# Performance work log

Measured on AMD Instinct MI355X. Metric: run time of the kernel, lower is better.

The kernel has to match this reference:

```python
import jax, jax.numpy as jnp
import numpy as np

L = 2048      # sequence length (self.len)
DIM = 1024    # model dim
DPOS = 128    # positional encoding dim
B = 4
EPS = 1e-5


def make_pe(length, d):
    # standard sinusoidal positional encoding, shape [length, d]
    pos = np.arange(length)[:, None].astype(np.float32)
    div = np.exp(-np.arange(0, d, 2).astype(np.float32) * (np.log(10000.0) / d))
    pe = np.zeros((length, d), dtype=np.float32)
    pe[:, 0::2] = np.sin(pos * div)
    pe[:, 1::2] = np.cos(pos * div)
    return jnp.asarray(pe)


def setup_inputs() -> dict:
    key = jax.random.key(0)
    ks = jax.random.split(key, 16)
    s = lambda fan_in: 1.0 / np.sqrt(fan_in)
    inp = {
        "z": jax.random.normal(ks[0], (B, L, DIM), jnp.float32),
        "x": jax.random.normal(ks[1], (B, L, DIM), jnp.float32),
        "a": jax.random.normal(ks[2], (1,), jnp.float32),
        "pe": make_pe(L, DPOS),
        # torch Linear weights stored [out, in]
        "w_pos1": jax.random.normal(ks[3], (DPOS + DIM, DPOS), jnp.float32) * s(DPOS),
        "b_pos1": jnp.zeros((DPOS + DIM,), jnp.float32),
        "w_pos2": jax.random.normal(ks[4], (DIM, DPOS + DIM), jnp.float32) * s(DPOS + DIM),
        "b_pos2": jnp.zeros((DIM,), jnp.float32),
        "w1": jax.random.normal(ks[5], (DIM * 2, DIM), jnp.float32) * s(DIM),
        "b1": jnp.zeros((DIM * 2,), jnp.float32),
        "w2": jax.random.normal(ks[6], (DIM, DIM * 2), jnp.float32) * s(DIM * 2),
        "b2": jnp.zeros((DIM,), jnp.float32),
        "w3": jax.random.normal(ks[7], (DIM * 2, DIM), jnp.float32) * s(DIM),
        "b3": jnp.zeros((DIM * 2,), jnp.float32),
        "w4": jax.random.normal(ks[8], (DIM, DIM * 2), jnp.float32) * s(DIM * 2),
        "b4": jnp.zeros((DIM,), jnp.float32),
        "ln_g": jnp.ones((DIM,), jnp.float32),
        "ln_b": jnp.zeros((DIM,), jnp.float32),
    }
    return inp


def _layer_norm(v, g, b):
    mu = jnp.mean(v, axis=-1, keepdims=True)
    var = jnp.var(v, axis=-1, keepdims=True)
    return (v - mu) * jax.lax.rsqrt(var + EPS) * g + b


def _lin(v, w, b):
    return v @ w.T + b


def reference(z, x, a, pe, w_pos1, b_pos1, w_pos2, b_pos2,
              w1, b1, w2, b2, w3, b3, w4, b4, ln_g, ln_b):
    zn = _layer_norm(z, ln_g, ln_b)                       # [B, L, D]
    fz = jnp.fft.rfft(zn, n=2 * L, axis=1)                # [B, L+1, D] complex
    expa = jnp.exp(a)                                     # [1]
    window = jnp.exp(-jnp.arange(L, dtype=jnp.float32) * expa)  # [L]
    h = _lin(pe, w_pos1, b_pos1)                          # [L, DPOS+D]
    h = jax.nn.gelu(h, approximate=False)
    h = _lin(h, w_pos2, b_pos2)                           # [L, D] (dropout eval = id)
    wfh = jnp.fft.rfft(window[:, None] * h, n=2 * L, axis=0)  # [L+1, D]
    cwhz = jnp.fft.irfft(wfh * fz, axis=1)[:, :L, :]      # [B, L, D]
    x1 = _lin(x, w1, b1)
    x1 = jax.nn.gelu(x1, approximate=False)
    x1 = _lin(x1, w2, b2)
    x1 = x1 * cwhz + z
    y = _layer_norm(x1, ln_g, ln_b)
    y = _lin(y, w3, b3)
    y = jax.nn.gelu(y, approximate=False)
    y = _lin(y, w4, b4)
    return y + x1
```

## Files before the change

kernel.cpp:

```cpp
#include <hip/hip_runtime.h>
#include <hip/hip_bf16.h>
#include <cmath>

typedef __hip_bfloat16 bf16;
typedef __attribute__((ext_vector_type(8))) short bf16x8;
typedef __attribute__((ext_vector_type(4))) float f32x4;

static __device__ __forceinline__ float b2f(bf16 v) { return __bfloat162float(v); }
static __device__ __forceinline__ bf16 f2b(float v) { return __float2bfloat16(v); }
static __device__ __forceinline__ float us2f(unsigned short u) {
  return __uint_as_float(((unsigned)u) << 16);
}

static __device__ __forceinline__ void gl2lds16(const bf16* g, bf16* l) {
  __builtin_amdgcn_global_load_lds(
      (const __attribute__((address_space(1))) void*)g,
      (__attribute__((address_space(3))) void*)l, 16, 0, 0);
}

static __device__ __forceinline__ float gelu_fast(float v) {
  float u = v * (0.7978845608f + 0.0356774081f * v * v);
  float e = __expf(2.f * u);
  return v * (e * __frcp_rn(e + 1.f));
}

struct CvtSegs { const float* src[7]; int blk_off[8]; };
__global__ __launch_bounds__(256) void cvt7_k(CvtSegs s, bf16* __restrict__ dst0)
{
  int b = blockIdx.x;
  int seg = 0;
#pragma unroll
  for (int i = 0; i < 6; ++i) seg += (b >= s.blk_off[i + 1]) ? 1 : 0;
  const float* src = s.src[seg] + (size_t)(b - s.blk_off[seg]) * 1024;
  bf16* dst = dst0 + (size_t)b * 1024;
  int idx = threadIdx.x * 4;
  float4 v = *(const float4*)(src + idx);
  union { bf16 bb[4]; ushort4 u; } o;
  o.bb[0] = f2b(v.x); o.bb[1] = f2b(v.y); o.bb[2] = f2b(v.z); o.bb[3] = f2b(v.w);
  *(ushort4*)(dst + idx) = o.u;
}

__global__ __launch_bounds__(256) void cvt_k(const float* __restrict__ in,
                                             bf16* __restrict__ out, int n)
{
  int idx = (blockIdx.x * 256 + threadIdx.x) * 4;
  if (idx >= n) return;
  float4 v = *(const float4*)(in + idx);
  union { bf16 b[4]; ushort4 u; } o;
  o.b[0] = f2b(v.x); o.b[1] = f2b(v.y); o.b[2] = f2b(v.z); o.b[3] = f2b(v.w);
  *(ushort4*)(out + idx) = o.u;
}

__global__ __launch_bounds__(256) void ln_k(const float* __restrict__ X, bf16* __restrict__ Y,
                                            const float* __restrict__ gamma,
                                            const float* __restrict__ beta)
{
  __shared__ float red[16];
  const int row = blockIdx.x, tid = threadIdx.x;
  float4 v = *(const float4*)(X + (size_t)row * 1024 + tid * 4);
  float s  = v.x + v.y + v.z + v.w;
  float s2 = v.x * v.x + v.y * v.y + v.z * v.z + v.w * v.w;
#pragma unroll
  for (int m = 32; m; m >>= 1) { s += __shfl_xor(s, m, 64); s2 += __shfl_xor(s2, m, 64); }
  const int wid = tid >> 6;
  if ((tid & 63) == 0) { red[wid] = s; red[wid + 8] = s2; }
  __syncthreads();
  s  = red[0] + red[1] + red[2] + red[3];
  s2 = red[8] + red[9] + red[10] + red[11];
  const float mu  = s * (1.f / 1024.f);
  const float var = s2 * (1.f / 1024.f) - mu * mu;
  const float rs  = rsqrtf(var + 1e-5f);
  float4 g = *(const float4*)(gamma + tid * 4);
  float4 bt = *(const float4*)(beta + tid * 4);
  union { bf16 b[4]; ushort4 u; } o;
  o.b[0] = f2b((v.x - mu) * rs * g.x + bt.x);
  o.b[1] = f2b((v.y - mu) * rs * g.y + bt.y);
  o.b[2] = f2b((v.z - mu) * rs * g.z + bt.z);
  o.b[3] = f2b((v.w - mu) * rs * g.w + bt.w);
  *(ushort4*)(Y + (size_t)row * 1024 + tid * 4) = o.u;
}

template<int EPI>
__global__ __launch_bounds__(256, 3) void gemm_k(
    const bf16* __restrict__ A, const bf16* __restrict__ W,
    const float* __restrict__ bias, void* __restrict__ Out,
    const void* __restrict__ aux0, const void* __restrict__ aux1,
    int M, int N, int K)
{
  __shared__ bf16 As[3][128 * 32];
  __shared__ bf16 Bs[3][128 * 32];
  const int tid = threadIdx.x;
  const int wid = tid >> 6, lane = tid & 63;
  const int quad = lane >> 4, l16 = lane & 15;
  const int wm = wid >> 1, wn = wid & 1;

  const int nwg = gridDim.x * gridDim.y;
  int lid = blockIdx.y * gridDim.x + blockIdx.x;
  {
    const int q = nwg >> 3, r = nwg & 7;
    const int xcd = lid & 7, loc = lid >> 3;
    const int base = (xcd < r) ? xcd * (q + 1) : r * (q + 1) + (xcd - r) * q;
    lid = base + loc;
  }
  const int bx = lid % gridDim.x, by = lid / gridDim.x;
  const int m0 = by * 128, n0 = bx * 128;

  f32x4 acc[4][4];
#pragma unroll
  for (int i = 0; i < 4; ++i)
#pragma unroll
    for (int j = 0; j < 4; ++j) acc[i][j] = (f32x4){0.f, 0.f, 0.f, 0.f};

  const bf16 *ga[2], *gb[2];
  int ldso[2];
#pragma unroll
  for (int r = 0; r < 2; ++r) {
    int p = r * 256 + wid * 64 + lane;
    int row = p >> 2;
    int sko = ((p & 3) ^ ((p >> 3) & 3)) << 3;
    ga[r] = A + (size_t)(m0 + row) * K + sko;
    gb[r] = W + (size_t)(n0 + row) * K + sko;
    ldso[r] = (r * 256 + wid * 64) * 8;
  }
  int apos[4], bpos[4];
#pragma unroll
  for (int i = 0; i < 4; ++i) {
    int ar = wm * 64 + i * 16 + l16;
    apos[i] = (ar * 4 + (quad ^ ((ar >> 1) & 3))) * 8;
    int br = wn * 64 + i * 16 + l16;
    bpos[i] = (br * 4 + (quad ^ ((br >> 1) & 3))) * 8;
  }

  const int niter = K >> 5;
#pragma unroll
  for (int t = 0; t < 2; ++t)
#pragma unroll
    for (int r = 0; r < 2; ++r) {
      gl2lds16(ga[r] + t * 32, &As[t][ldso[r]]);
      gl2lds16(gb[r] + t * 32, &Bs[t][ldso[r]]);
    }

  int cur = 0;
  for (int k = 0; k < niter; ++k) {
    if (k == niter - 1) { asm volatile("s_waitcnt vmcnt(0)" ::: "memory"); }
    else               { asm volatile("s_waitcnt vmcnt(4)" ::: "memory"); }
    asm volatile("s_barrier" ::: "memory");

    const bf16* as = As[cur];
    const bf16* bs = Bs[cur];
    bf16x8 af[4], bfr[4];
#pragma unroll
    for (int i = 0; i < 4; ++i) af[i]  = *(const bf16x8*)(as + apos[i]);
#pragma unroll
    for (int j = 0; j < 4; ++j) bfr[j] = *(const bf16x8*)(bs + bpos[j]);
    asm volatile("s_waitcnt lgkmcnt(0)" ::: "memory");

    if (k + 2 < niter) {
      int nb = cur + 2; if (nb >= 3) nb -= 3;
#pragma unroll
      for (int r = 0; r < 2; ++r) {
        gl2lds16(ga[r] + (k + 2) * 32, &As[nb][ldso[r]]);
        gl2lds16(gb[r] + (k + 2) * 32, &Bs[nb][ldso[r]]);
      }
    }
#pragma unroll
    for (int i = 0; i < 4; ++i)
#pragma unroll
      for (int j = 0; j < 4; ++j)
        acc[i][j] = __builtin_amdgcn_mfma_f32_16x16x32_bf16(af[i], bfr[j], acc[i][j], 0, 0, 0);
    cur += 1; if (cur == 3) cur = 0;
  }

  float expa = 0.f;
  if (EPI == 1) expa = expf(((const float*)aux0)[0]);
#pragma unroll
  for (int i = 0; i < 4; ++i) {
    const int gm_base = m0 + wm * 64 + i * 16 + quad * 4;
#pragma unroll
    for (int j = 0; j < 4; ++j) {
      const int gn = n0 + wn * 64 + j * 16 + l16;
      const float bv = bias[gn];
#pragma unroll
      for (int r = 0; r < 4; ++r) {
        const int gm = gm_base + r;
        const size_t off = (size_t)gm * N + gn;
        float v = acc[i][j][r] + bv;
        if (EPI == 0) ((bf16*)Out)[off] = f2b(gelu_fast(v));
        else if (EPI == 1) ((float*)Out)[off] = v * expf(-(float)gm * expa);
        else if (EPI == 2) ((float*)Out)[off] = v * ((const float*)aux0)[off] + ((const float*)aux1)[off];
        else ((float*)Out)[off] = v + ((const float*)aux0)[off];
      }
    }
  }
}

__global__ __launch_bounds__(256) void conv_k(
    const bf16* __restrict__ zn,
    const float* __restrict__ wh,
    const float* __restrict__ a,
    float* __restrict__ out)
{
  __shared__ float whs[64 * 64];
  __shared__ float znt[128 * 64];
  const int tid = threadIdx.x;
  const int dd = tid & 63, ttg = tid >> 6;
  const int t0 = blockIdx.x * 64, d0 = blockIdx.y * 64, b = blockIdx.z;
  const float expa = expf(a[0]);
  const float smax = 20.7f / expa;
  const unsigned short* znu = (const unsigned short*)zn;

  float acc[16];
#pragma unroll
  for (int q = 0; q < 16; ++q) acc[q] = 0.f;

  for (int sb = 0; sb <= t0 + 63; sb += 64) {
    if ((float)sb > smax) break;
    float4 wv4[4];
#pragma unroll
    for (int i = 0; i < 4; ++i) {
      int cc = tid + 256 * i;
      int row = cc >> 4, dq = (cc & 15) * 4;
      wv4[i] = *(const float4*)&wh[(size_t)(sb + row) * 1024 + d0 + dq];
    }
    ushort4 zv4[8];
#pragma unroll
    for (int i = 0; i < 8; ++i) {
      int cc = tid + 256 * i;
      int row = cc >> 4, dq = (cc & 15) * 4;
      int u = t0 - sb - 64 + row;
      zv4[i] = (u >= 0) ? *(const ushort4*)&znu[((size_t)b * 2048 + u) * 1024 + d0 + dq]
                        : make_ushort4(0, 0, 0, 0);
    }
#pragma unroll
    for (int i = 0; i < 4; ++i) {
      int cc = tid + 256 * i;
      *(float4*)&whs[(cc >> 4) * 64 + (cc & 15) * 4] = wv4[i];
    }
#pragma unroll
    for (int i = 0; i < 8; ++i) {
      int cc = tid + 256 * i;
      float4 o;
      o.x = us2f(zv4[i].x); o.y = us2f(zv4[i].y); o.z = us2f(zv4[i].z); o.w = us2f(zv4[i].w);
      *(float4*)&znt[(cc >> 4) * 64 + (cc & 15) * 4] = o;
    }
    __syncthreads();

    float win[16];
#pragma unroll
    for (int q = 0; q < 16; ++q) win[q] = znt[(ttg * 16 + q + 64) * 64 + dd];
#pragma unroll
    for (int ss = 0; ss < 64; ++ss) {
      float wv = whs[ss * 64 + dd];
#pragma unroll
      for (int q = 0; q < 16; ++q) acc[q] += wv * win[q];
      if (ss < 63) {
#pragma unroll
        for (int q = 15; q >= 1; --q) win[q] = win[q - 1];
        win[0] = znt[(ttg * 16 + 63 - ss) * 64 + dd];
      }
    }
    __syncthreads();
  }
#pragma unroll
  for (int q = 0; q < 16; ++q) {
    int t = t0 + ttg * 16 + q;
    out[((size_t)b * 2048 + t) * 1024 + d0 + dd] = acc[q];
  }
}

extern "C" void kernel_launch(void* const* d_in, const int* in_sizes, int n_in,
                              void* d_out, int out_size, void* d_ws, size_t ws_size,
                              hipStream_t stream)
{
  const float* z      = (const float*)d_in[0];
  const float* x      = (const float*)d_in[1];
  const float* a      = (const float*)d_in[2];
  const float* pe     = (const float*)d_in[3];
  const float* w_pos1 = (const float*)d_in[4];
  const float* b_pos1 = (const float*)d_in[5];
  const float* w_pos2 = (const float*)d_in[6];
  const float* b_pos2 = (const float*)d_in[7];
  const float* w1     = (const float*)d_in[8];
  const float* b1     = (const float*)d_in[9];
  const float* w2     = (const float*)d_in[10];
  const float* b2     = (const float*)d_in[11];
  const float* w3     = (const float*)d_in[12];
  const float* b3     = (const float*)d_in[13];
  const float* w4     = (const float*)d_in[14];
  const float* b4     = (const float*)d_in[15];
  const float* ln_g   = (const float*)d_in[16];
  const float* ln_b   = (const float*)d_in[17];

  char* ws = (char*)d_ws;
  bf16* pe_bf  = (bf16*)(ws + 0);
  bf16* wp1_bf = (bf16*)(ws + 524288);
  bf16* wp2_bf = (bf16*)(ws + 819200);
  bf16* w1_bf  = (bf16*)(ws + 3178496);
  bf16* w2_bf  = (bf16*)(ws + 7372800);
  bf16* w3_bf  = (bf16*)(ws + 11567104);
  bf16* w4_bf  = (bf16*)(ws + 15761408);
  bf16* h1     = (bf16*)(ws + 19955712);
  bf16* zn_bf  = (bf16*)(ws + 24674304);
  bf16* x_bf   = (bf16*)(ws + 41451520);
  float* wh    = (float*)(ws + 58228736);
  float* cwhz  = (float*)(ws + 66617344);
  bf16*  x1n   = (bf16*)(ws + 66617344);
  bf16*  g     = (bf16*)(ws + 100171776);
  float* x1    = (float*)(ws + 24674304);
  float* out   = (float*)d_out;

  CvtSegs segs;
  segs.src[0] = pe;  segs.src[1] = w_pos1; segs.src[2] = w_pos2;
  segs.src[3] = w1;  segs.src[4] = w2;     segs.src[5] = w3; segs.src[6] = w4;
  int bo[8] = {0, 256, 400, 1552, 3600, 5648, 7696, 9744};
  for (int i = 0; i < 8; ++i) segs.blk_off[i] = bo[i];
  cvt7_k<<<9744, 256, 0, stream>>>(segs, (bf16*)ws);
  cvt_k<<<8192, 256, 0, stream>>>(x, x_bf, 8388608);

  ln_k<<<8192, 256, 0, stream>>>(z, zn_bf, ln_g, ln_b);
  gemm_k<0><<<dim3(9, 16), 256, 0, stream>>>(pe_bf, wp1_bf, b_pos1, h1, nullptr, nullptr, 2048, 1152, 128);
  gemm_k<1><<<dim3(8, 16), 256, 0, stream>>>(h1, wp2_bf, b_pos2, wh, a, nullptr, 2048, 1024, 1152);
  conv_k<<<dim3(32, 16, 4), 256, 0, stream>>>(zn_bf, wh, a, cwhz);
  gemm_k<0><<<dim3(16, 64), 256, 0, stream>>>(x_bf, w1_bf, b1, g, nullptr, nullptr, 8192, 2048, 1024);
  gemm_k<2><<<dim3(8, 64), 256, 0, stream>>>(g, w2_bf, b2, x1, cwhz, z, 8192, 1024, 2048);
  ln_k<<<8192, 256, 0, stream>>>(x1, x1n, ln_g, ln_b);
  gemm_k<0><<<dim3(16, 64), 256, 0, stream>>>(x1n, w3_bf, b3, g, nullptr, nullptr, 8192, 2048, 1024);
  gemm_k<3><<<dim3(8, 64), 256, 0, stream>>>(g, w4_bf, b4, out, x1, nullptr, 8192, 1024, 2048);
}
```

Baseline: 418.3 us.

## Add 256x256-tile 8-wave GEMM kernel for the two up-projection GEMMs

Introduces a new GEMM kernel with 512 threads, 256x256 output tiles, K-step 64, and double-buffered LDS filled via global_load_lds. The MFMA work is interleaved with barriers and s_setprio in a ping-pong schedule. It replaces the 128x128 kernel for the two 8192x2048x1024 GEMMs with GELU epilogue, aiming for higher data reuse per tile and better overlap of loads with compute. The trade-offs are much higher register and LDS use (128KB LDS), fewer workgroups (256), and scalar bf16 stores in the epilogue.

```diff
diff --git a/kernel.cpp b/kernel.cpp
--- a/kernel.cpp
+++ b/kernel.cpp
@@ -78,6 +78,131 @@
   o.b[2] = f2b((v.z - mu) * rs * g.z + bt.z);
   o.b[3] = f2b((v.w - mu) * rs * g.w + bt.w);
   *(ushort4*)(Y + (size_t)row * 1024 + tid * 4) = o.u;
+}
+
+template<int EPI>
+__global__ __launch_bounds__(512, 2) void gemm8p_k(
+    const bf16* __restrict__ A, const bf16* __restrict__ W,
+    const float* __restrict__ bias, void* __restrict__ Out,
+    int M, int N, int K)
+{
+  __shared__ bf16 lds[65536];
+  const int tid = threadIdx.x;
+  const int wid = tid >> 6, lane = tid & 63;
+  const int quad = lane >> 4, l16 = lane & 15;
+  const int wm = wid >> 2, wn = wid & 3;
+
+  const int nwg = gridDim.x * gridDim.y;
+  int lid = blockIdx.y * gridDim.x + blockIdx.x;
+  {
+    const int q = nwg >> 3, r = nwg & 7;
+    const int xcd = lid & 7, loc = lid >> 3;
+    const int base = (xcd < r) ? xcd * (q + 1) : r * (q + 1) + (xcd - r) * q;
+    lid = base + loc;
+  }
+  const int bx = lid % gridDim.x, by = lid / gridDim.x;
+  const int m0 = by * 256, n0 = bx * 256;
+
+  f32x4 acc[8][4];
+#pragma unroll
+  for (int i = 0; i < 8; ++i)
+#pragma unroll
+    for (int j = 0; j < 4; ++j) acc[i][j] = (f32x4){0.f, 0.f, 0.f, 0.f};
+
+  const int aoff0 = wm * 8192 + quad * 1024 + l16 * 8;
+  const int boff0 = (wn >> 1) * 8192 + quad * 1024 + (wn & 1) * 512 + l16 * 8;
+
+  const int NT = K >> 6;
+
+#define STAGE_TILE(t)                                                              \
+  {                                                                                \
+    bf16* asl = lds + ((t) & 1) * 16384;                                           \
+    bf16* bsl = lds + 32768 + ((t) & 1) * 16384;                                   \
+    const size_t ko = (size_t)(t) * 64 + wid * 8;                                  \
+    _Pragma("unroll")                                                              \
+    for (int H = 0; H < 2; ++H)                                                    \
+      _Pragma("unroll")                                                            \
+      for (int h = 0; h < 2; ++h) {                                                \
+        gl2lds16(A + (size_t)(m0 + H * 128 + h * 64 + lane) * K + ko,              \
+                 asl + H * 8192 + wid * 1024 + h * 512);                           \
+        gl2lds16(W + (size_t)(n0 + H * 128 + h * 64 + lane) * K + ko,              \
+                 bsl + H * 8192 + wid * 1024 + h * 512);                           \
+      }                                                                            \
+  }
+
+  STAGE_TILE(0);
+  asm volatile("s_waitcnt vmcnt(0)" ::: "memory");
+  asm volatile("s_barrier" ::: "memory");
+
+  for (int T = 0; T < NT; ++T) {
+    const bf16* as = lds + (T & 1) * 16384;
+    const bf16* bs = lds + 32768 + (T & 1) * 16384;
+    bf16x8 bf[4][2];
+    bf16x8 af[2][2];
+
+#pragma unroll
+    for (int nf = 0; nf < 4; ++nf)
+#pragma unroll
+      for (int ks = 0; ks < 2; ++ks)
+        bf[nf][ks] = *(const bf16x8*)(bs + boff0 + ks * 4096 + nf * 128);
+#pragma unroll
+    for (int i = 0; i < 2; ++i)
+#pragma unroll
+      for (int ks = 0; ks < 2; ++ks)
+        af[i][ks] = *(const bf16x8*)(as + aoff0 + ks * 4096 + i * 128);
+    if (T + 1 < NT) STAGE_TILE(T + 1);
+    asm volatile("s_barrier" ::: "memory");
+    asm volatile("s_waitcnt lgkmcnt(0)" ::: "memory");
+    __builtin_amdgcn_s_setprio(1);
+#pragma unroll
+    for (int nf = 0; nf < 4; ++nf)
+#pragma unroll
+      for (int i = 0; i < 2; ++i)
+#pragma unroll
+        for (int ks = 0; ks < 2; ++ks)
+          acc[i][nf] = __builtin_amdgcn_mfma_f32_16x16x32_bf16(af[i][ks], bf[nf][ks], acc[i][nf], 0, 0, 0);
+    __builtin_amdgcn_s_setprio(0);
+    asm volatile("s_barrier" ::: "memory");
+
+#pragma unroll
+    for (int q = 1; q < 4; ++q) {
+#pragma unroll
+      for (int i = 0; i < 2; ++i)
+#pragma unroll
+        for (int ks = 0; ks < 2; ++ks)
+          af[i][ks] = *(const bf16x8*)(as + aoff0 + ks * 4096 + (2 * q + i) * 128);
+      if (q == 3) { asm volatile("s_waitcnt vmcnt(0)" ::: "memory"); }
+      asm volatile("s_barrier" ::: "memory");
+      asm volatile("s_waitcnt lgkmcnt(0)" ::: "memory");
+      __builtin_amdgcn_s_setprio(1);
+#pragma unroll
+      for (int nf = 0; nf < 4; ++nf)
+#pragma unroll
+        for (int i = 0; i < 2; ++i)
+#pragma unroll
+          for (int ks = 0; ks < 2; ++ks)
+            acc[2 * q + i][nf] = __builtin_amdgcn_mfma_f32_16x16x32_bf16(af[i][ks], bf[nf][ks], acc[2 * q + i][nf], 0, 0, 0);
+      __builtin_amdgcn_s_setprio(0);
+      asm volatile("s_barrier" ::: "memory");
+    }
+  }
+#undef STAGE_TILE
+
+#pragma unroll
+  for (int mf = 0; mf < 8; ++mf) {
+    const int gm_base = m0 + wm * 128 + mf * 16 + quad * 4;
+#pragma unroll
+    for (int nf = 0; nf < 4; ++nf) {
+      const int gn = n0 + wn * 64 + nf * 16 + l16;
+      const float bv = bias[gn];
+#pragma unroll
+      for (int r = 0; r < 4; ++r) {
+        const size_t off = (size_t)(gm_base + r) * N + gn;
+        float v = acc[mf][nf][r] + bv;
+        ((bf16*)Out)[off] = f2b(gelu_fast(v));
+      }
+    }
+  }
 }
 
 template<int EPI>
@@ -321,9 +446,9 @@
   gemm_k<0><<<dim3(9, 16), 256, 0, stream>>>(pe_bf, wp1_bf, b_pos1, h1, nullptr, nullptr, 2048, 1152, 128);
   gemm_k<1><<<dim3(8, 16), 256, 0, stream>>>(h1, wp2_bf, b_pos2, wh, a, nullptr, 2048, 1024, 1152);
   conv_k<<<dim3(32, 16, 4), 256, 0, stream>>>(zn_bf, wh, a, cwhz);
-  gemm_k<0><<<dim3(16, 64), 256, 0, stream>>>(x_bf, w1_bf, b1, g, nullptr, nullptr, 8192, 2048, 1024);
+  gemm8p_k<0><<<dim3(8, 32), 512, 0, stream>>>(x_bf, w1_bf, b1, g, 8192, 2048, 1024);
   gemm_k<2><<<dim3(8, 64), 256, 0, stream>>>(g, w2_bf, b2, x1, cwhz, z, 8192, 1024, 2048);
   ln_k<<<8192, 256, 0, stream>>>(x1, x1n, ln_g, ln_b);
-  gemm_k<0><<<dim3(16, 64), 256, 0, stream>>>(x1n, w3_bf, b3, g, nullptr, nullptr, 8192, 2048, 1024);
+  gemm8p_k<0><<<dim3(8, 32), 512, 0, stream>>>(x1n, w3_bf, b3, g, 8192, 2048, 1024);
   gemm_k<3><<<dim3(8, 64), 256, 0, stream>>>(g, w4_bf, b4, out, x1, nullptr, 8192, 1024, 2048);
 }
```

Result: slower. 439.2 us (+5.0%).

## Use larger 256-row tiles with 512-thread blocks for the four big GEMMs

Applied to the files above, without the earlier changes.

Adds two GEMM kernels with 512 threads per block and a three-slot pipeline that loads directly from global memory into LDS. The up-projection uses 256x256 tiles and the down-projection uses 256x128 tiles. Both replace the 128x128 kernel for the four large FFN GEMMs, raising data reuse per block and cutting redundant global/L2 traffic. The new LDS layout drops the XOR swizzle, which may add bank conflicts. The grids shrink to 256 blocks, which lowers wave-count flexibility and may cost occupancy. The XCD swizzle is factored into a helper.

```diff
diff --git a/kernel.cpp b/kernel.cpp
--- a/kernel.cpp
+++ b/kernel.cpp
@@ -22,6 +22,13 @@
   float u = v * (0.7978845608f + 0.0356774081f * v * v);
   float e = __expf(2.f * u);
   return v * (e * __frcp_rn(e + 1.f));
+}
+
+static __device__ __forceinline__ int xcd_swz(int lid, int nwg) {
+  const int q = nwg >> 3, r = nwg & 7;
+  const int xcd = lid & 7, loc = lid >> 3;
+  const int base = (xcd < r) ? xcd * (q + 1) : r * (q + 1) + (xcd - r) * q;
+  return base + loc;
 }
 
 struct CvtSegs { const float* src[7]; int blk_off[8]; };
@@ -80,6 +87,199 @@
   *(ushort4*)(Y + (size_t)row * 1024 + tid * 4) = o.u;
 }
 
+__global__ __launch_bounds__(512, 2) void gemm3sa_k(
+    const bf16* __restrict__ A, const bf16* __restrict__ W,
+    const float* __restrict__ bias, bf16* __restrict__ Out,
+    int M, int N, int K)
+{
+  __shared__ bf16 lds[49152];
+  const int tid = threadIdx.x;
+  const int wid = tid >> 6, lane = tid & 63;
+  const int quad = lane >> 4, l16 = lane & 15;
+  const int wm = wid >> 2, wn = wid & 3;
+
+  const int nwg = gridDim.x * gridDim.y;
+  int lid = xcd_swz(blockIdx.y * gridDim.x + blockIdx.x, nwg);
+  const int bx = lid % gridDim.x, by = lid / gridDim.x;
+  const int m0 = by * 256, n0 = bx * 256;
+
+  f32x4 acc[8][4];
+#pragma unroll
+  for (int i = 0; i < 8; ++i)
+#pragma unroll
+    for (int j = 0; j < 4; ++j) acc[i][j] = (f32x4){0.f, 0.f, 0.f, 0.f};
+
+  const bf16 *ga[2], *gb[2];
+  int ldso[2];
+#pragma unroll
+  for (int r = 0; r < 2; ++r) {
+    const int row = (wid & 3) * 64 + lane;
+    const int ch  = 2 * r + (wid >> 2);
+    ga[r] = A + (size_t)(m0 + row) * K + ch * 8;
+    gb[r] = W + (size_t)(n0 + row) * K + ch * 8;
+    ldso[r] = (r * 512 + wid * 64) * 8;
+  }
+  const int aofs = quad * 2048 + wm * 1024 + l16 * 8;
+  const int bofs = quad * 2048 + wn * 512 + l16 * 8;
+
+  const int niter = K >> 5;
+
+#define STAGE_A(kk, slot)                                                   \
+  {                                                                         \
+    bf16* asl = lds + (slot) * 8192;                                        \
+    bf16* bsl = lds + 24576 + (slot) * 8192;                                \
+    _Pragma("unroll")                                                       \
+    for (int r = 0; r < 2; ++r) {                                           \
+      gl2lds16(ga[r] + (kk) * 32, asl + ldso[r]);                           \
+      gl2lds16(gb[r] + (kk) * 32, bsl + ldso[r]);                           \
+    }                                                                       \
+  }
+
+  STAGE_A(0, 0);
+  STAGE_A(1, 1);
+
+  int cur = 0;
+  for (int k = 0; k < niter; ++k) {
+    if (k == niter - 1) { asm volatile("s_waitcnt vmcnt(0)" ::: "memory"); }
+    else               { asm volatile("s_waitcnt vmcnt(4)" ::: "memory"); }
+    asm volatile("s_barrier" ::: "memory");
+
+    const bf16* as = lds + cur * 8192;
+    const bf16* bs = lds + 24576 + cur * 8192;
+    bf16x8 bfr[4], af[8];
+#pragma unroll
+    for (int nf = 0; nf < 4; ++nf) bfr[nf] = *(const bf16x8*)(bs + bofs + nf * 128);
+#pragma unroll
+    for (int mf = 0; mf < 8; ++mf) af[mf]  = *(const bf16x8*)(as + aofs + mf * 128);
+
+    if (k + 2 < niter) {
+      int nb = cur + 2; if (nb >= 3) nb -= 3;
+      STAGE_A(k + 2, nb);
+    }
+#pragma unroll
+    for (int mf = 0; mf < 8; ++mf)
+#pragma unroll
+      for (int nf = 0; nf < 4; ++nf)
+        acc[mf][nf] = __builtin_amdgcn_mfma_f32_16x16x32_bf16(af[mf], bfr[nf], acc[mf][nf], 0, 0, 0);
+    cur += 1; if (cur == 3) cur = 0;
+  }
+#undef STAGE_A
+
+#pragma unroll
+  for (int mf = 0; mf < 8; ++mf) {
+    const int gm_base = m0 + wm * 128 + mf * 16 + quad * 4;
+#pragma unroll
+    for (int nf = 0; nf < 4; ++nf) {
+      const int gn = n0 + wn * 64 + nf * 16 + l16;
+      const float bv = bias[gn];
+#pragma unroll
+      for (int r = 0; r < 4; ++r) {
+        const size_t off = (size_t)(gm_base + r) * N + gn;
+        Out[off] = f2b(gelu_fast(acc[mf][nf][r] + bv));
+      }
+    }
+  }
+}
+
+template<int EPI>
+__global__ __launch_bounds__(512, 2) void gemm3sb_k(
+    const bf16* __restrict__ A, const bf16* __restrict__ W,
+    const float* __restrict__ bias, float* __restrict__ Out,
+    const float* __restrict__ aux0, const float* __restrict__ aux1,
+    int M, int N, int K)
+{
+  __shared__ bf16 lds[36864];
+  const int tid = threadIdx.x;
+  const int wid = tid >> 6, lane = tid & 63;
+  const int quad = lane >> 4, l16 = lane & 15;
+  const int wm = wid >> 1, wn = wid & 1;
+
+  const int nwg = gridDim.x * gridDim.y;
+  int lid = xcd_swz(blockIdx.y * gridDim.x + blockIdx.x, nwg);
+  const int bx = lid % gridDim.x, by = lid / gridDim.x;
+  const int m0 = by * 256, n0 = bx * 128;
+
+  f32x4 acc[4][4];
+#pragma unroll
+  for (int i = 0; i < 4; ++i)
+#pragma unroll
+    for (int j = 0; j < 4; ++j) acc[i][j] = (f32x4){0.f, 0.f, 0.f, 0.f};
+
+  const bf16 *ga[2], *gbp;
+  int ldsoA[2];
+#pragma unroll
+  for (int r = 0; r < 2; ++r) {
+    const int row = (wid & 3) * 64 + lane;
+    const int ch  = 2 * r + (wid >> 2);
+    ga[r] = A + (size_t)(m0 + row) * K + ch * 8;
+    ldsoA[r] = (r * 512 + wid * 64) * 8;
+  }
+  gbp = W + (size_t)(n0 + (wid & 1) * 64 + lane) * K + (wid >> 1) * 8;
+  const int ldsoB = wid * 512;
+
+  const int aofs = quad * 2048 + wm * 512 + l16 * 8;
+  const int bofs = quad * 1024 + wn * 512 + l16 * 8;
+
+  const int niter = K >> 5;
+
+#define STAGE_B(kk, slot)                                                   \
+  {                                                                         \
+    bf16* asl = lds + (slot) * 8192;                                        \
+    bf16* bsl = lds + 24576 + (slot) * 4096;                                \
+    _Pragma("unroll")                                                       \
+    for (int r = 0; r < 2; ++r)                                             \
+      gl2lds16(ga[r] + (kk) * 32, asl + ldsoA[r]);                          \
+    gl2lds16(gbp + (kk) * 32, bsl + ldsoB);                                 \
+  }
+
+  STAGE_B(0, 0);
+  STAGE_B(1, 1);
+
+  int cur = 0;
+  for (int k = 0; k < niter; ++k) {
+    if (k == niter - 1) { asm volatile("s_waitcnt vmcnt(0)" ::: "memory"); }
+    else               { asm volatile("s_waitcnt vmcnt(3)" ::: "memory"); }
+    asm volatile("s_barrier" ::: "memory");
+
+    const bf16* as = lds + cur * 8192;
+    const bf16* bs = lds + 24576 + cur * 4096;
+    bf16x8 bfr[4], af[4];
+#pragma unroll
+    for (int nf = 0; nf < 4; ++nf) bfr[nf] = *(const bf16x8*)(bs + bofs + nf * 128);
+#pragma unroll
+    for (int mf = 0; mf < 4; ++mf) af[mf]  = *(const bf16x8*)(as + aofs + mf * 128);
+
+    if (k + 2 < niter) {
+      int nb = cur + 2; if (nb >= 3) nb -= 3;
+      STAGE_B(k + 2, nb);
+    }
+#pragma unroll
+    for (int mf = 0; mf < 4; ++mf)
+#pragma unroll
+      for (int nf = 0; nf < 4; ++nf)
+        acc[mf][nf] = __builtin_amdgcn_mfma_f32_16x16x32_bf16(af[mf], bfr[nf], acc[mf][nf], 0, 0, 0);
+    cur += 1; if (cur == 3) cur = 0;
+  }
+#undef STAGE_B
+
+#pragma unroll
+  for (int mf = 0; mf < 4; ++mf) {
+    const int gm_base = m0 + wm * 64 + mf * 16 + quad * 4;
+#pragma unroll
+    for (int nf = 0; nf < 4; ++nf) {
+      const int gn = n0 + wn * 64 + nf * 16 + l16;
+      const float bv = bias[gn];
+#pragma unroll
+      for (int r = 0; r < 4; ++r) {
+        const size_t off = (size_t)(gm_base + r) * N + gn;
+        float v = acc[mf][nf][r] + bv;
+        if (EPI == 2) Out[off] = v * aux0[off] + aux1[off];
+        else          Out[off] = v + aux0[off];
+      }
+    }
+  }
+}
+
 template<int EPI>
 __global__ __launch_bounds__(256, 3) void gemm_k(
     const bf16* __restrict__ A, const bf16* __restrict__ W,
@@ -95,13 +295,7 @@
   const int wm = wid >> 1, wn = wid & 1;
 
   const int nwg = gridDim.x * gridDim.y;
-  int lid = blockIdx.y * gridDim.x + blockIdx.x;
-  {
-    const int q = nwg >> 3, r = nwg & 7;
-    const int xcd = lid & 7, loc = lid >> 3;
-    const int base = (xcd < r) ? xcd * (q + 1) : r * (q + 1) + (xcd - r) * q;
-    lid = base + loc;
-  }
+  int lid = xcd_swz(blockIdx.y * gridDim.x + blockIdx.x, nwg);
   const int bx = lid % gridDim.x, by = lid / gridDim.x;
   const int m0 = by * 128, n0 = bx * 128;
 
@@ -321,9 +515,9 @@
   gemm_k<0><<<dim3(9, 16), 256, 0, stream>>>(pe_bf, wp1_bf, b_pos1, h1, nullptr, nullptr, 2048, 1152, 128);
   gemm_k<1><<<dim3(8, 16), 256, 0, stream>>>(h1, wp2_bf, b_pos2, wh, a, nullptr, 2048, 1024, 1152);
   conv_k<<<dim3(32, 16, 4), 256, 0, stream>>>(zn_bf, wh, a, cwhz);
-  gemm_k<0><<<dim3(16, 64), 256, 0, stream>>>(x_bf, w1_bf, b1, g, nullptr, nullptr, 8192, 2048, 1024);
-  gemm_k<2><<<dim3(8, 64), 256, 0, stream>>>(g, w2_bf, b2, x1, cwhz, z, 8192, 1024, 2048);
+  gemm3sa_k<<<dim3(8, 32), 512, 0, stream>>>(x_bf, w1_bf, b1, g, 8192, 2048, 1024);
+  gemm3sb_k<2><<<dim3(8, 32), 512, 0, stream>>>(g, w2_bf, b2, x1, cwhz, z, 8192, 1024, 2048);
   ln_k<<<8192, 256, 0, stream>>>(x1, x1n, ln_g, ln_b);
-  gemm_k<0><<<dim3(16, 64), 256, 0, stream>>>(x1n, w3_bf, b3, g, nullptr, nullptr, 8192, 2048, 1024);
-  gemm_k<3><<<dim3(8, 64), 256, 0, stream>>>(g, w4_bf, b4, out, x1, nullptr, 8192, 1024, 2048);
-}
+  gemm3sa_k<<<dim3(8, 32), 512, 0, stream>>>(x1n, w3_bf, b3, g, 8192, 2048, 1024);
+  gemm3sb_k<3><<<dim3(8, 32), 512, 0, stream>>>(g, w4_bf, b4, out, x1, nullptr, 8192, 1024, 2048);
+}
```

Result: slower. 528.0 us (+26.2%).
